# Kernel optimization log

Hardware: AMD Instinct MI355X
Metric: run time of the kernel (lower is better)

The kernel has to match this reference:

```python
import jax, jax.numpy as jnp
import numpy as np

N = 80000          # total nodes
F_IN = 16          # num_features
NUM_GRAPHS = 8
P = N // NUM_GRAPHS
EDGES_PER_GRAPH = 80000   # undirected samples per graph (~avg degree 16 after symmetrize)
OUT_DIM = 20000    # num_nodes (output classes)


def _graclus(src, dst, n, rng):
    """Greedy graclus matching (unweighted): visit nodes in random order, match with
    first unmatched neighbor. Cluster id = min(i, match[i]), relabeled consecutively."""
    perm = np.argsort(src, kind='stable')
    s, d = src[perm], dst[perm]
    starts = np.searchsorted(s, np.arange(n))
    ends = np.searchsorted(s, np.arange(n) + 1)
    match = np.full(n, -1, dtype=np.int64)
    for u in rng.permutation(n):
        if match[u] >= 0:
            continue
        match[u] = u
        for v in d[starts[u]:ends[u]]:
            if v != u and match[v] < 0:
                match[u] = v
                match[v] = u
                break
    rep = np.minimum(np.arange(n), match)
    _, cluster = np.unique(rep, return_inverse=True)
    return cluster.astype(np.int64)


def _pool_edges(src, dst, cluster, n1):
    """max_pool edge pooling: map endpoints to clusters, drop self-loops, coalesce."""
    cs, cd = cluster[src], cluster[dst]
    m = cs != cd
    key = np.unique(cs[m].astype(np.int64) * n1 + cd[m])
    return (key // n1).astype(np.int64), (key % n1).astype(np.int64)


def _glorot(k, shape):
    return jax.random.normal(k, shape, jnp.float32) * (2.0 / (shape[0] + shape[1])) ** 0.5


def setup_inputs() -> dict:
    rng = np.random.default_rng(0)
    srcs, dsts = [], []
    for g in range(NUM_GRAPHS):  # edges only within each graph block
        lo = g * P
        u = rng.integers(0, P, EDGES_PER_GRAPH)
        v = rng.integers(0, P, EDGES_PER_GRAPH)
        m = u != v
        u, v = u[m] + lo, v[m] + lo
        key = np.unique(np.minimum(u, v).astype(np.int64) * N + np.maximum(u, v))
        a, b = key // N, key % N
        srcs += [a, b]
        dsts += [b, a]
    src = np.concatenate(srcs).astype(np.int64)
    dst = np.concatenate(dsts).astype(np.int64)
    batch1 = (np.arange(N) // P).astype(np.int64)

    cluster1 = _graclus(src, dst, N, rng)
    n1 = int(cluster1.max()) + 1
    src2, dst2 = _pool_edges(src, dst, cluster1, n1)
    batch2 = np.zeros(n1, np.int64)
    batch2[cluster1] = batch1
    cluster2 = _graclus(src2, dst2, n1, rng)
    n2 = int(cluster2.max()) + 1
    batch3 = np.zeros(n2, np.int64)
    batch3[cluster2] = batch2

    ks = jax.random.split(jax.random.key(0), 12)
    return dict(
        x=jax.random.normal(ks[0], (N, F_IN), jnp.float32),
        W0a=_glorot(ks[1], (F_IN, 32)), W1a=_glorot(ks[2], (F_IN, 32)),
        b1=jnp.zeros((32,), jnp.float32),
        W0b=_glorot(ks[3], (32, 64)), W1b=_glorot(ks[4], (32, 64)),
        b2=jnp.zeros((64,), jnp.float32),
        fcw1=_glorot(ks[5], (64, 128)), fcb1=jnp.zeros((128,), jnp.float32),
        fcw2=_glorot(ks[6], (128, OUT_DIM)), fcb2=jnp.zeros((OUT_DIM,), jnp.float32),
        edge_index1=jnp.asarray(np.stack([src, dst])),
        cluster1=jnp.asarray(cluster1),
        edge_index2=jnp.asarray(np.stack([src2, dst2])),
        cluster2=jnp.asarray(cluster2),
        batch3=jnp.asarray(batch3),
        n1=n1, n2=n2, n_graphs=NUM_GRAPHS,
    )


def _cheb_relu(x, edge_index, W0, W1, b, n):
    """PyG ChebConv K=2, sym norm, lambda_max=2: out = x@W0 + (L~ x)@W1 + b with
    L~ = L - I = -D^{-1/2} A D^{-1/2}; then ReLU."""
    s, d = edge_index[0], edge_index[1]
    deg = jax.ops.segment_sum(jnp.ones(s.shape[0], x.dtype), d, num_segments=n)
    dinv = jnp.where(deg > 0, deg ** -0.5, 0.0)
    w = -(dinv[s] * dinv[d])                       # [E]
    tx1 = jax.ops.segment_sum(w[:, None] * x[s], d, num_segments=n)  # L~ x
    return jax.nn.relu(x @ W0 + tx1 @ W1 + b)


def reference(x, W0a, W1a, b1, W0b, W1b, b2, fcw1, fcb1, fcw2, fcb2,
              edge_index1, cluster1, edge_index2, cluster2, batch3,
              n1, n2, n_graphs):
    h = _cheb_relu(x, edge_index1, W0a, W1a, b1, x.shape[0])     # [N,32]
    hp = jax.ops.segment_max(h, cluster1, num_segments=n1)        # max_pool -> [n1,32]
    h2 = _cheb_relu(hp, edge_index2, W0b, W1b, b2, n1)            # [n1,64]
    h3 = jax.ops.segment_max(h2, cluster2, num_segments=n2)       # max_pool_x -> [n2,64]
    sums = jax.ops.segment_sum(h3, batch3, num_segments=n_graphs)
    cnt = jax.ops.segment_sum(jnp.ones(h3.shape[0], h3.dtype), batch3, num_segments=n_graphs)
    g = sums / cnt[:, None]                                       # global_mean_pool [G,64]
    g = jax.nn.relu(g @ fcw1 + fcb1)                              # dropout is eval-mode identity
    return g @ fcw2 + fcb2                                        # [G, OUT_DIM]
```

## Files before the change

### kernel.cpp

```cpp
#include <hip/hip_runtime.h>

static inline int idiv(int a, int b) { return (a + b - 1) / b; }

__device__ __forceinline__ int swz8(int bid, int nb) {
    int q = nb >> 3, r = nb & 7;
    int x = bid & 7, c = bid >> 3;
    return (x < r ? x * (q + 1) : r * (q + 1) + (x - r) * q) + c;
}

__global__ void k_zero(float4* __restrict__ p, long n4) {
    long t = (long)blockIdx.x * blockDim.x + threadIdx.x;
    long stride = (long)gridDim.x * blockDim.x;
    for (; t < n4; t += stride) p[t] = make_float4(0.f, 0.f, 0.f, 0.f);
}

__global__ void k_prep1(const int* __restrict__ src, const int* __restrict__ dst,
                        int* __restrict__ ust, int* __restrict__ uen,
                        int* __restrict__ cntS, int E) {
    int e = blockIdx.x * blockDim.x + threadIdx.x;
    if (e >= E) return;
    int s = src[e], d = dst[e];
    if (s >= d) return;
    atomicAdd(&cntS[d], 1);
    bool prevup = false; int ps = -1;
    if (e > 0) { ps = src[e - 1]; prevup = (ps < dst[e - 1]); }
    if (e == 0 || !prevup || ps != s) ust[s] = e;
    bool nextup = false; int ns = -1;
    if (e + 1 < E) { ns = src[e + 1]; nextup = (ns < dst[e + 1]); }
    if (e + 1 == E || !nextup || ns != s) uen[s] = e + 1;
}

__global__ void k_bounds2(const int* __restrict__ src, int* __restrict__ rs,
                          int* __restrict__ re, int E) {
    int e = blockIdx.x * blockDim.x + threadIdx.x;
    if (e >= E) return;
    int s = src[e];
    if (e == 0 || src[e - 1] != s) rs[s] = e;
    if (e + 1 == E || src[e + 1] != s) re[s] = e + 1;
}

__global__ void k_dinv2(const int* __restrict__ rs, const int* __restrict__ re,
                        float* __restrict__ dinv, int n) {
    int t = blockIdx.x * blockDim.x + threadIdx.x;
    if (t < n) {
        int deg = re[t] - rs[t];
        dinv[t] = (deg > 0) ? rsqrtf((float)deg) : 0.0f;
    }
}

__global__ void k_scan_blk(const int* __restrict__ cnt, int* __restrict__ offs,
                           int* __restrict__ blksum, int n) {
    __shared__ int ts[256];
    int blk = blockIdx.x;
    int tid = threadIdx.x;
    int i0 = blk * 1024 + tid * 4;
    int a0 = 0, a1 = 0, a2 = 0, a3 = 0;
    if (i0 + 3 < n) {
        int4 v = *(const int4*)&cnt[i0];
        a0 = v.x; a1 = v.y; a2 = v.z; a3 = v.w;
    } else {
        if (i0 + 0 < n) a0 = cnt[i0 + 0];
        if (i0 + 1 < n) a1 = cnt[i0 + 1];
        if (i0 + 2 < n) a2 = cnt[i0 + 2];
    }
    int tsum = a0 + a1 + a2 + a3;
    ts[tid] = tsum;
    __syncthreads();
    for (int off = 1; off < 256; off <<= 1) {
        int v = (tid >= off) ? ts[tid - off] : 0;
        __syncthreads();
        ts[tid] += v;
        __syncthreads();
    }
    int ex = ts[tid] - tsum;
    if (tid == 255) blksum[blk] = ts[255];
    int p0 = ex, p1 = ex + a0, p2 = p1 + a1, p3 = p2 + a2;
    if (i0 + 3 < n) {
        *(int4*)&offs[i0] = make_int4(p0, p1, p2, p3);
    } else {
        if (i0 + 0 < n) offs[i0 + 0] = p0;
        if (i0 + 1 < n) offs[i0 + 1] = p1;
        if (i0 + 2 < n) offs[i0 + 2] = p2;
    }
}

__global__ void k_scan_tot(int* __restrict__ blksum, int nblk) {
    __shared__ int s[1024];
    int tid = threadIdx.x;
    int v = (tid < nblk) ? blksum[tid] : 0;
    s[tid] = v;
    __syncthreads();
    for (int off = 1; off < 1024; off <<= 1) {
        int t = (tid >= off) ? s[tid - off] : 0;
        __syncthreads();
        s[tid] += t;
        __syncthreads();
    }
    if (tid < nblk) blksum[tid] = s[tid] - v;
}

__global__ void k_scan_add_dinv(int* __restrict__ offs, int* __restrict__ cursor,
                                const int* __restrict__ blksum, const int* __restrict__ cntS,
                                const int* __restrict__ ust, const int* __restrict__ uen,
                                float* __restrict__ dinv, int n) {
    int t = blockIdx.x * blockDim.x + threadIdx.x;
    if (t < n) {
        int v = offs[t] + blksum[t >> 10];
        offs[t] = v;
        cursor[t] = v;
        int deg = cntS[t] + uen[t] - ust[t];
        dinv[t] = (deg > 0) ? rsqrtf((float)deg) : 0.0f;
    }
}

__global__ void k_fillS(const int* __restrict__ src, const int* __restrict__ dst,
                        int* __restrict__ cursor, int* __restrict__ csr, int E) {
    int e = blockIdx.x * blockDim.x + threadIdx.x;
    if (e >= E) return;
    int s = src[e], d = dst[e];
    if (s < d) {
        int pos = atomicAdd(&cursor[d], 1);
        csr[pos] = s;
    }
}

template <int LOGF>
__global__ void k_gather1(const int* __restrict__ ust, const int* __restrict__ uen,
                          const int* __restrict__ dst1, const int* __restrict__ offsS,
                          const int* __restrict__ cntS, const int* __restrict__ csrS,
                          const float* __restrict__ dinv, const float* __restrict__ xin,
                          float* __restrict__ tx, int n) {
    int vb = swz8(blockIdx.x, gridDim.x);
    int t = vb * blockDim.x + threadIdx.x;
    int d = t >> LOGF, f = t & ((1 << LOGF) - 1);
    if (d >= n) return;
    float acc = 0.0f;
    int e = ust[d], e1 = uen[d];
    for (; e + 3 < e1; e += 4) {
        int s0 = dst1[e], s1 = dst1[e + 1], s2 = dst1[e + 2], s3 = dst1[e + 3];
        float v0 = dinv[s0] * xin[((long)s0 << LOGF) + f];
        float v1 = dinv[s1] * xin[((long)s1 << LOGF) + f];
        float v2 = dinv[s2] * xin[((long)s2 << LOGF) + f];
        float v3 = dinv[s3] * xin[((long)s3 << LOGF) + f];
        acc += (v0 + v1) + (v2 + v3);
    }
    for (; e < e1; e++) {
        int s = dst1[e];
        acc += dinv[s] * xin[((long)s << LOGF) + f];
    }
    int i = offsS[d], i1 = i + cntS[d];
    for (; i + 3 < i1; i += 4) {
        int s0 = csrS[i], s1 = csrS[i + 1], s2 = csrS[i + 2], s3 = csrS[i + 3];
        float v0 = dinv[s0] * xin[((long)s0 << LOGF) + f];
        float v1 = dinv[s1] * xin[((long)s1 << LOGF) + f];
        float v2 = dinv[s2] * xin[((long)s2 << LOGF) + f];
        float v3 = dinv[s3] * xin[((long)s3 << LOGF) + f];
        acc += (v0 + v1) + (v2 + v3);
    }
    for (; i < i1; i++) {
        int s = csrS[i];
        acc += dinv[s] * xin[((long)s << LOGF) + f];
    }
    tx[((long)d << LOGF) + f] = -dinv[d] * acc;
}

template <int LOGF>
__global__ void k_gather2(const int* __restrict__ rs, const int* __restrict__ re,
                          const int* __restrict__ dst2, const float* __restrict__ dinv,
                          const float* __restrict__ xin, float* __restrict__ tx, int n) {
    int vb = swz8(blockIdx.x, gridDim.x);
    int t = vb * blockDim.x + threadIdx.x;
    int d = t >> LOGF, f = t & ((1 << LOGF) - 1);
    if (d >= n) return;
    float acc = 0.0f;
    int j = rs[d], j1 = re[d];
    for (; j + 3 < j1; j += 4) {
        int s0 = dst2[j], s1 = dst2[j + 1], s2 = dst2[j + 2], s3 = dst2[j + 3];
        float v0 = dinv[s0] * xin[((long)s0 << LOGF) + f];
        float v1 = dinv[s1] * xin[((long)s1 << LOGF) + f];
        float v2 = dinv[s2] * xin[((long)s2 << LOGF) + f];
        float v3 = dinv[s3] * xin[((long)s3 << LOGF) + f];
        acc += (v0 + v1) + (v2 + v3);
    }
    for (; j < j1; j++) {
        int s = dst2[j];
        acc += dinv[s] * xin[((long)s << LOGF) + f];
    }
    tx[((long)d << LOGF) + f] = -dinv[d] * acc;
}

__global__ void k_cheb1_max(const float* __restrict__ x, const float* __restrict__ tx,
                            const float* __restrict__ W0, const float* __restrict__ W1,
                            const float* __restrict__ b, const int* __restrict__ cl,
                            float* __restrict__ hp, int N) {
    int t = blockIdx.x * blockDim.x + threadIdx.x;
    int n = t >> 5, j = t & 31;
    if (n >= N) return;
    const float* xr = x + (long)n * 16;
    const float* tr = tx + (long)n * 16;
    float acc = b[j];
#pragma unroll
    for (int k = 0; k < 16; k++) acc += xr[k] * W0[k * 32 + j] + tr[k] * W1[k * 32 + j];
    float v = fmaxf(acc, 0.0f);
    atomicMax((int*)&hp[((long)cl[n] << 5) + j], __float_as_int(v));
}

__global__ void k_cheb2_max(const float* __restrict__ xp, const float* __restrict__ tx,
                            const float* __restrict__ W0, const float* __restrict__ W1,
                            const float* __restrict__ b, const int* __restrict__ cl,
                            float* __restrict__ h3, int n1) {
    int t = blockIdx.x * blockDim.x + threadIdx.x;
    int n = t >> 6, j = t & 63;
    if (n >= n1) return;
    const float* xr = xp + (long)n * 32;
    const float* tr = tx + (long)n * 32;
    float acc = b[j];
#pragma unroll
    for (int k = 0; k < 32; k++) acc += xr[k] * W0[k * 64 + j] + tr[k] * W1[k * 64 + j];
    float v = fmaxf(acc, 0.0f);
    atomicMax((int*)&h3[((long)cl[n] << 6) + j], __float_as_int(v));
}

__global__ void k_gsum(const float* __restrict__ h3, const int* __restrict__ batch,
                       float* __restrict__ gsum, float* __restrict__ gcnt, int n2) {
    __shared__ float s[8 * 64];
    __shared__ float sc[8];
    for (int i = threadIdx.x; i < 512; i += blockDim.x) s[i] = 0.0f;
    if (threadIdx.x < 8) sc[threadIdx.x] = 0.0f;
    __syncthreads();
    long total = (long)n2 * 64;
    long stride = (long)gridDim.x * blockDim.x;
    for (long t = (long)blockIdx.x * blockDim.x + threadIdx.x; t < total; t += stride) {
        int n = (int)(t >> 6), f = (int)(t & 63);
        int g = batch[n];
        atomicAdd(&s[g * 64 + f], h3[t]);
        if (f == 0) atomicAdd(&sc[g], 1.0f);
    }
    __syncthreads();
    for (int i = threadIdx.x; i < 512; i += blockDim.x) atomicAdd(&gsum[i], s[i]);
    if (threadIdx.x < 8) atomicAdd(&gcnt[threadIdx.x], sc[threadIdx.x]);
}

__global__ void k_fc1(const float* __restrict__ gsum, const float* __restrict__ gcnt,
                      const float* __restrict__ fcw1, const float* __restrict__ fcb1,
                      float* __restrict__ g1) {
    __shared__ float sg[8 * 64];
    int tid = threadIdx.x;
    if (tid < 512) {
        float c = gcnt[tid >> 6];
        sg[tid] = (c > 0.0f) ? gsum[tid] / c : 0.0f;
    }
    __syncthreads();
    int gi = tid >> 7, j = tid & 127;
    float acc = fcb1[j];
#pragma unroll 8
    for (int k = 0; k < 64; k++) acc += sg[gi * 64 + k] * fcw1[k * 128 + j];
    g1[tid] = fmaxf(acc, 0.0f);
}

__global__ void k_fc2(const float* __restrict__ g1, const float* __restrict__ fcw2,
                      const float* __restrict__ fcb2, float* __restrict__ out, int OUT) {
    __shared__ float sg[8 * 128];
    for (int i = threadIdx.x; i < 1024; i += blockDim.x) sg[i] = g1[i];
    __syncthreads();
    int o = blockIdx.x * blockDim.x + threadIdx.x;
    if (o >= OUT) return;
    float bias = fcb2[o];
    float acc[8];
#pragma unroll
    for (int gi = 0; gi < 8; gi++) acc[gi] = bias;
    for (int k = 0; k < 128; k++) {
        float w = fcw2[(long)k * OUT + o];
#pragma unroll
        for (int gi = 0; gi < 8; gi++) acc[gi] += sg[gi * 128 + k] * w;
    }
#pragma unroll
    for (int gi = 0; gi < 8; gi++) out[(long)gi * OUT + o] = acc[gi];
}

extern "C" void kernel_launch(void* const* d_in, const int* in_sizes, int n_in,
                              void* d_out, int out_size, void* d_ws, size_t ws_size,
                              hipStream_t stream) {
    const float* x    = (const float*)d_in[0];
    const float* W0a  = (const float*)d_in[1];
    const float* W1a  = (const float*)d_in[2];
    const float* b1   = (const float*)d_in[3];
    const float* W0b  = (const float*)d_in[4];
    const float* W1b  = (const float*)d_in[5];
    const float* b2   = (const float*)d_in[6];
    const float* fcw1 = (const float*)d_in[7];
    const float* fcb1 = (const float*)d_in[8];
    const float* fcw2 = (const float*)d_in[9];
    const float* fcb2 = (const float*)d_in[10];
    const int* ei1    = (const int*)d_in[11];
    const int* cl1    = (const int*)d_in[12];
    const int* ei2    = (const int*)d_in[13];
    const int* cl2    = (const int*)d_in[14];
    const int* b3     = (const int*)d_in[15];

    const int N  = in_sizes[12];
    const int E1 = in_sizes[11] / 2;
    const int E2 = in_sizes[13] / 2;
    const int n1 = in_sizes[14];
    const int n2 = in_sizes[15];
    const int G  = 8;
    const int OUT = out_size / G;

    const int nmax = (N > n1) ? N : n1;

    auto rnd = [](size_t b) { return (b + 255) & ~(size_t)255; };
    size_t cntB  = rnd((size_t)N * 4);
    size_t ustB  = rnd((size_t)N * 4);
    size_t uenB  = rnd((size_t)N * 4);
    size_t rs2B  = rnd((size_t)n1 * 4);
    size_t re2B  = rnd((size_t)n1 * 4);
    size_t hpB   = rnd((size_t)n1 * 32 * 4);
    size_t h3B   = rnd((size_t)n2 * 64 * 4);
    size_t smlB  = rnd((512 + 8 + 1024) * 4);
    size_t offB  = rnd((size_t)N * 4);
    size_t curB  = rnd((size_t)N * 4);
    size_t csrB  = rnd((size_t)(E1 / 2 + 64) * 4);
    size_t dinvB = rnd((size_t)nmax * 4);
    size_t blkB  = rnd((size_t)1024 * 4);

    char* base = (char*)d_ws;
    char* p = base;
    int*   cntS   = (int*)p;           p += cntB;
    int*   ust    = (int*)p;           p += ustB;
    int*   uen    = (int*)p;           p += uenB;
    int*   rs2    = (int*)p;           p += rs2B;
    int*   re2    = (int*)p;           p += re2B;
    float* hp     = (float*)p;         p += hpB;
    float* h3     = (float*)p;         p += h3B;
    float* gsum   = (float*)p;         p += smlB;
    float* gcnt   = gsum + 512;
    float* g1     = gcnt + 8;
    size_t zeroB  = (size_t)(p - base);
    int*   offsS  = (int*)p;           p += offB;
    int*   cursorS= (int*)p;           p += curB;
    int*   csrS   = (int*)p;           p += csrB;
    float* dinv   = (float*)p;         p += dinvB;
    int*   blksum = (int*)p;           p += blkB;
    float* txA    = (float*)p;
    (void)ws_size;

    dim3 B(256);
    {
        long n4 = (long)(zeroB / 16);
        int g = idiv((int)((n4 < 1048576) ? n4 : 1048576), 256);
        if (g < 1) g = 1;
        if (g > 4096) g = 4096;
        k_zero<<<g, B, 0, stream>>>((float4*)base, n4);
    }

    {
        int nblk = idiv(N, 1024);
        k_prep1<<<idiv(E1, 256), B, 0, stream>>>(ei1, ei1 + E1, ust, uen, cntS, E1);
        k_scan_blk<<<nblk, B, 0, stream>>>(cntS, offsS, blksum, N);
        k_scan_tot<<<1, 1024, 0, stream>>>(blksum, nblk);
        k_scan_add_dinv<<<idiv(N, 256), B, 0, stream>>>(offsS, cursorS, blksum, cntS, ust, uen,
                                                        dinv, N);
        k_fillS<<<idiv(E1, 256), B, 0, stream>>>(ei1, ei1 + E1, cursorS, csrS, E1);
        k_gather1<4><<<idiv(N * 16, 256), B, 0, stream>>>(ust, uen, ei1 + E1, offsS, cntS, csrS,
                                                          dinv, x, txA, N);
        k_cheb1_max<<<idiv(N * 32, 256), B, 0, stream>>>(x, txA, W0a, W1a, b1, cl1, hp, N);
    }

    {
        k_bounds2<<<idiv(E2, 256), B, 0, stream>>>(ei2, rs2, re2, E2);
        k_dinv2<<<idiv(n1, 256), B, 0, stream>>>(rs2, re2, dinv, n1);
        k_gather2<5><<<idiv(n1 * 32, 256), B, 0, stream>>>(rs2, re2, ei2 + E2, dinv, hp, txA, n1);
        k_cheb2_max<<<idiv(n1 * 64, 256), B, 0, stream>>>(hp, txA, W0b, W1b, b2, cl2, h3, n1);
    }

    int gb = idiv(n2 * 64, 256);
    if (gb > 256) gb = 256;
    k_gsum<<<gb, B, 0, stream>>>(h3, b3, gsum, gcnt, n2);
    k_fc1<<<1, 1024, 0, stream>>>(gsum, gcnt, fcw1, fcb1, g1);
    k_fc2<<<idiv(OUT, 256), B, 0, stream>>>(g1, fcw2, fcb2, (float*)d_out, OUT);
}
```

Measured before the change: 228.5 us.

## Replace atomicMax pooling with precomputed cluster member lists and gather-max

Builds per-cluster member lists (at most two members, as in graclus matching) with a counting kernel. The Chebyshev layers then write dense outputs, and separate pooling passes gather and max over the members, replacing scattered float atomicMax. This trades contended atomics for extra kernels, an extra intermediate buffer and additional global memory traffic. It assumes every cluster has at most two members, which holds for graclus.

```diff
diff --git a/kernel.cpp b/kernel.cpp
--- a/kernel.cpp
+++ b/kernel.cpp
@@ -46,6 +46,15 @@
         int deg = re[t] - rs[t];
         dinv[t] = (deg > 0) ? rsqrtf((float)deg) : 0.0f;
     }
+}
+
+__global__ void k_members(const int* __restrict__ cl, int* __restrict__ mcnt,
+                          int* __restrict__ mem, int n) {
+    int t = blockIdx.x * blockDim.x + threadIdx.x;
+    if (t >= n) return;
+    int c = cl[t];
+    int slot = atomicAdd(&mcnt[c], 1);
+    if (slot < 2) mem[2 * c + slot] = t;
 }
 
 __global__ void k_scan_blk(const int* __restrict__ cnt, int* __restrict__ offs,
@@ -189,10 +198,9 @@
     tx[((long)d << LOGF) + f] = -dinv[d] * acc;
 }
 
-__global__ void k_cheb1_max(const float* __restrict__ x, const float* __restrict__ tx,
-                            const float* __restrict__ W0, const float* __restrict__ W1,
-                            const float* __restrict__ b, const int* __restrict__ cl,
-                            float* __restrict__ hp, int N) {
+__global__ void k_cheb1(const float* __restrict__ x, const float* __restrict__ tx,
+                        const float* __restrict__ W0, const float* __restrict__ W1,
+                        const float* __restrict__ b, float* __restrict__ h, int N) {
     int t = blockIdx.x * blockDim.x + threadIdx.x;
     int n = t >> 5, j = t & 31;
     if (n >= N) return;
@@ -201,14 +209,26 @@
     float acc = b[j];
 #pragma unroll
     for (int k = 0; k < 16; k++) acc += xr[k] * W0[k * 32 + j] + tr[k] * W1[k * 32 + j];
-    float v = fmaxf(acc, 0.0f);
-    atomicMax((int*)&hp[((long)cl[n] << 5) + j], __float_as_int(v));
-}
-
-__global__ void k_cheb2_max(const float* __restrict__ xp, const float* __restrict__ tx,
-                            const float* __restrict__ W0, const float* __restrict__ W1,
-                            const float* __restrict__ b, const int* __restrict__ cl,
-                            float* __restrict__ h3, int n1) {
+    h[t] = fmaxf(acc, 0.0f);
+}
+
+__global__ void k_pool1(const int* __restrict__ mcnt, const int* __restrict__ mem,
+                        const float* __restrict__ h, float* __restrict__ hp, int n1) {
+    int t = blockIdx.x * blockDim.x + threadIdx.x;
+    int c = t >> 5, j = t & 31;
+    if (c >= n1) return;
+    int m0 = mem[2 * c];
+    float v = h[((long)m0 << 5) + j];
+    if (mcnt[c] > 1) {
+        int m1 = mem[2 * c + 1];
+        v = fmaxf(v, h[((long)m1 << 5) + j]);
+    }
+    hp[t] = v;
+}
+
+__global__ void k_cheb2(const float* __restrict__ xp, const float* __restrict__ tx,
+                        const float* __restrict__ W0, const float* __restrict__ W1,
+                        const float* __restrict__ b, float* __restrict__ h2, int n1) {
     int t = blockIdx.x * blockDim.x + threadIdx.x;
     int n = t >> 6, j = t & 63;
     if (n >= n1) return;
@@ -217,12 +237,12 @@
     float acc = b[j];
 #pragma unroll
     for (int k = 0; k < 32; k++) acc += xr[k] * W0[k * 64 + j] + tr[k] * W1[k * 64 + j];
-    float v = fmaxf(acc, 0.0f);
-    atomicMax((int*)&h3[((long)cl[n] << 6) + j], __float_as_int(v));
-}
-
-__global__ void k_gsum(const float* __restrict__ h3, const int* __restrict__ batch,
-                       float* __restrict__ gsum, float* __restrict__ gcnt, int n2) {
+    h2[t] = fmaxf(acc, 0.0f);
+}
+
+__global__ void k_gsum2(const float* __restrict__ h2, const int* __restrict__ mcnt,
+                        const int* __restrict__ mem, const int* __restrict__ batch,
+                        float* __restrict__ gsum, float* __restrict__ gcnt, int n2) {
     __shared__ float s[8 * 64];
     __shared__ float sc[8];
     for (int i = threadIdx.x; i < 512; i += blockDim.x) s[i] = 0.0f;
@@ -231,9 +251,15 @@
     long total = (long)n2 * 64;
     long stride = (long)gridDim.x * blockDim.x;
     for (long t = (long)blockIdx.x * blockDim.x + threadIdx.x; t < total; t += stride) {
-        int n = (int)(t >> 6), f = (int)(t & 63);
-        int g = batch[n];
-        atomicAdd(&s[g * 64 + f], h3[t]);
+        int c = (int)(t >> 6), f = (int)(t & 63);
+        int m0 = mem[2 * c];
+        float v = h2[((long)m0 << 6) + f];
+        if (mcnt[c] > 1) {
+            int m1 = mem[2 * c + 1];
+            v = fmaxf(v, h2[((long)m1 << 6) + f]);
+        }
+        int g = batch[c];
+        atomicAdd(&s[g * 64 + f], v);
         if (f == 0) atomicAdd(&sc[g], 1.0f);
     }
     __syncthreads();
@@ -307,6 +333,8 @@
     const int OUT = out_size / G;
 
     const int nmax = (N > n1) ? N : n1;
+    long hElems = (long)N * 32;
+    if ((long)n1 * 64 > hElems) hElems = (long)n1 * 64;
 
     auto rnd = [](size_t b) { return (b + 255) & ~(size_t)255; };
     size_t cntB  = rnd((size_t)N * 4);
@@ -314,14 +342,20 @@
     size_t uenB  = rnd((size_t)N * 4);
     size_t rs2B  = rnd((size_t)n1 * 4);
     size_t re2B  = rnd((size_t)n1 * 4);
-    size_t hpB   = rnd((size_t)n1 * 32 * 4);
-    size_t h3B   = rnd((size_t)n2 * 64 * 4);
+    size_t mc1B  = rnd((size_t)n1 * 4);
+    size_t mc2B  = rnd((size_t)n2 * 4);
     size_t smlB  = rnd((512 + 8 + 1024) * 4);
     size_t offB  = rnd((size_t)N * 4);
     size_t curB  = rnd((size_t)N * 4);
     size_t csrB  = rnd((size_t)(E1 / 2 + 64) * 4);
     size_t dinvB = rnd((size_t)nmax * 4);
     size_t blkB  = rnd((size_t)1024 * 4);
+    size_t mem1B = rnd((size_t)n1 * 2 * 4);
+    size_t mem2B = rnd((size_t)n2 * 2 * 4);
+    size_t hpB   = rnd((size_t)n1 * 32 * 4);
+    size_t txB   = rnd((size_t)(((long)N * 16 > (long)n1 * 32) ? (long)N * 16 : (long)n1 * 32) * 4);
+    size_t hB    = rnd((size_t)hElems * 4);
+    (void)hB;
 
     char* base = (char*)d_ws;
     char* p = base;
@@ -330,8 +364,8 @@
     int*   uen    = (int*)p;           p += uenB;
     int*   rs2    = (int*)p;           p += rs2B;
     int*   re2    = (int*)p;           p += re2B;
-    float* hp     = (float*)p;         p += hpB;
-    float* h3     = (float*)p;         p += h3B;
+    int*   mcnt1  = (int*)p;           p += mc1B;
+    int*   mcnt2  = (int*)p;           p += mc2B;
     float* gsum   = (float*)p;         p += smlB;
     float* gcnt   = gsum + 512;
     float* g1     = gcnt + 8;
@@ -341,7 +375,11 @@
     int*   csrS   = (int*)p;           p += csrB;
     float* dinv   = (float*)p;         p += dinvB;
     int*   blksum = (int*)p;           p += blkB;
-    float* txA    = (float*)p;
+    int*   mem1   = (int*)p;           p += mem1B;
+    int*   mem2   = (int*)p;           p += mem2B;
+    float* hp     = (float*)p;         p += hpB;
+    float* txA    = (float*)p;         p += txB;
+    float* hbuf   = (float*)p;
     (void)ws_size;
 
     dim3 B(256);
@@ -356,6 +394,7 @@
     {
         int nblk = idiv(N, 1024);
         k_prep1<<<idiv(E1, 256), B, 0, stream>>>(ei1, ei1 + E1, ust, uen, cntS, E1);
+        k_members<<<idiv(N, 256), B, 0, stream>>>(cl1, mcnt1, mem1, N);
         k_scan_blk<<<nblk, B, 0, stream>>>(cntS, offsS, blksum, N);
         k_scan_tot<<<1, 1024, 0, stream>>>(blksum, nblk);
         k_scan_add_dinv<<<idiv(N, 256), B, 0, stream>>>(offsS, cursorS, blksum, cntS, ust, uen,
@@ -363,19 +402,21 @@
         k_fillS<<<idiv(E1, 256), B, 0, stream>>>(ei1, ei1 + E1, cursorS, csrS, E1);
         k_gather1<4><<<idiv(N * 16, 256), B, 0, stream>>>(ust, uen, ei1 + E1, offsS, cntS, csrS,
                                                           dinv, x, txA, N);
-        k_cheb1_max<<<idiv(N * 32, 256), B, 0, stream>>>(x, txA, W0a, W1a, b1, cl1, hp, N);
+        k_cheb1<<<idiv(N * 32, 256), B, 0, stream>>>(x, txA, W0a, W1a, b1, hbuf, N);
+        k_pool1<<<idiv(n1 * 32, 256), B, 0, stream>>>(mcnt1, mem1, hbuf, hp, n1);
     }
 
     {
         k_bounds2<<<idiv(E2, 256), B, 0, stream>>>(ei2, rs2, re2, E2);
+        k_members<<<idiv(n1, 256), B, 0, stream>>>(cl2, mcnt2, mem2, n1);
         k_dinv2<<<idiv(n1, 256), B, 0, stream>>>(rs2, re2, dinv, n1);
         k_gather2<5><<<idiv(n1 * 32, 256), B, 0, stream>>>(rs2, re2, ei2 + E2, dinv, hp, txA, n1);
-        k_cheb2_max<<<idiv(n1 * 64, 256), B, 0, stream>>>(hp, txA, W0b, W1b, b2, cl2, h3, n1);
+        k_cheb2<<<idiv(n1 * 64, 256), B, 0, stream>>>(hp, txA, W0b, W1b, b2, hbuf, n1);
     }
 
     int gb = idiv(n2 * 64, 256);
     if (gb > 256) gb = 256;
-    k_gsum<<<gb, B, 0, stream>>>(h3, b3, gsum, gcnt, n2);
+    k_gsum2<<<gb, B, 0, stream>>>(hbuf, mcnt2, mem2, b3, gsum, gcnt, n2);
     k_fc1<<<1, 1024, 0, stream>>>(gsum, gcnt, fcw1, fcb1, g1);
     k_fc2<<<idiv(OUT, 256), B, 0, stream>>>(g1, fcw2, fcb2, (float*)d_out, OUT);
 }
```

Result: slower. 255.3 us (+11.7%).
